# Optimization experiments

Hardware: AMD Instinct MI355X
Metric: run time of the kernel (lower is better)

Reference implementation:

```python
import jax, jax.numpy as jnp
import numpy as np

D, H, K = 384, 6, 8

def _ln(x, g, b, eps=1e-5):
    mu = jnp.mean(x, axis=-1, keepdims=True)
    var = jnp.mean((x - mu) ** 2, axis=-1, keepdims=True)
    return (x - mu) * jax.lax.rsqrt(var + eps) * g + b

def setup_inputs() -> dict:
    key = jax.random.key(0)
    ks = jax.random.split(key, 20)
    B, N = 4, 2048
    s = 0.02
    inp = {
        'x': jax.random.normal(ks[0], (B, N, D), jnp.float32),
        'knn_index': jax.random.randint(ks[1], (B * K * N,), 0, B * N, jnp.int64),
        'ln1_g': jnp.ones((D,), jnp.float32),
        'ln1_b': jnp.zeros((D,), jnp.float32),
        'w_qkv': jax.random.normal(ks[2], (D, 3 * D), jnp.float32) * s,
        'w_proj': jax.random.normal(ks[3], (D, D), jnp.float32) * s,
        'b_proj': jnp.zeros((D,), jnp.float32),
        'w_knn': jax.random.normal(ks[4], (2 * D, D), jnp.float32) * s,
        'b_knn': jnp.zeros((D,), jnp.float32),
        'w_g1': jax.random.normal(ks[5], (2 * D, D), jnp.float32) * s,
        'b_g1': jnp.zeros((D,), jnp.float32),
        'w_g2': jax.random.normal(ks[6], (D, D), jnp.float32) * s,
        'b_g2': jnp.zeros((D,), jnp.float32),
        'ln2_g': jnp.ones((D,), jnp.float32),
        'ln2_b': jnp.zeros((D,), jnp.float32),
        'w_fc1': jax.random.normal(ks[7], (D, 4 * D), jnp.float32) * s,
        'b_fc1': jnp.zeros((4 * D,), jnp.float32),
        'w_fc2': jax.random.normal(ks[8], (4 * D, D), jnp.float32) * s,
        'b_fc2': jnp.zeros((D,), jnp.float32),
    }
    return inp

def reference(x, knn_index, ln1_g, ln1_b, w_qkv, w_proj, b_proj, w_knn, b_knn,
              w_g1, b_g1, w_g2, b_g2, ln2_g, ln2_b, w_fc1, b_fc1, w_fc2, b_fc2):
    B, N, _ = x.shape
    hd = D // H
    scale = hd ** -0.5
    nx = _ln(x, ln1_g, ln1_b)
    # --- self attention ---
    qkv = (nx @ w_qkv).reshape(B, N, 3, H, hd).transpose(2, 0, 3, 1, 4)  # [3,B,H,N,hd]
    q, k, v = qkv[0], qkv[1], qkv[2]
    attn = jax.nn.softmax(jnp.einsum('bhnd,bhmd->bhnm', q * scale, k), axis=-1)
    attn_out = jnp.einsum('bhnm,bhmd->bhnd', attn, v).transpose(0, 2, 1, 3).reshape(B, N, D)
    attn_out = attn_out @ w_proj + b_proj
    # --- EdgeConv-style graph feature: gather-concat-MLP-maxpool ---
    feat = nx.reshape(B * N, D)[knn_index].reshape(B, K, N, D)
    xe = jnp.broadcast_to(nx[:, None], (B, K, N, D))
    gf = jnp.concatenate([feat - xe, xe], axis=-1)  # [B,K,N,2D]
    knn_out = jnp.max(jax.nn.leaky_relu(gf @ w_knn + b_knn, 0.2), axis=1)  # [B,N,D]
    # --- salience gate ---
    gi = jnp.concatenate([attn_out, knn_out], axis=-1)
    gate = jax.nn.sigmoid(jax.nn.gelu(gi @ w_g1 + b_g1, approximate=False) @ w_g2 + b_g2)
    fused = (1 - gate) * attn_out + gate * knn_out
    x = x + fused
    # --- FFN ---
    h = jax.nn.gelu(_ln(x, ln2_g, ln2_b) @ w_fc1 + b_fc1, approximate=False)
    x = x + (h @ w_fc2 + b_fc2)
    return x
```

## Files before the change

### kernel.cpp

```cpp
#include <hip/hip_runtime.h>
#include <math.h>

typedef unsigned short u16;
typedef __attribute__((ext_vector_type(8))) short short8;
typedef __attribute__((ext_vector_type(4))) float floatx4;
typedef __attribute__((ext_vector_type(16))) float floatx16;
typedef __attribute__((ext_vector_type(4))) short sh4v;
typedef __attribute__((ext_vector_type(2))) unsigned uint2v;

union sh4u { sh4v v; u16 u[4]; };
union sh8u { short8 v; u16 u[8]; };
union sh8w { short8 v; unsigned w[4]; };

__device__ __forceinline__ floatx4 mfma16(short8 a, short8 b, floatx4 c) {
  return __builtin_amdgcn_mfma_f32_16x16x32_bf16(a, b, c, 0, 0, 0);
}
__device__ __forceinline__ floatx16 mfma32(short8 a, short8 b, floatx16 c) {
  return __builtin_amdgcn_mfma_f32_32x32x16_bf16(a, b, c, 0, 0, 0);
}

__device__ __forceinline__ floatx4 zero4() {
  floatx4 z = {0.f, 0.f, 0.f, 0.f};
  return z;
}
__device__ __forceinline__ floatx16 zero16() {
  floatx16 z;
#pragma unroll
  for (int i = 0; i < 16; i++) z[i] = 0.f;
  return z;
}

__device__ __forceinline__ u16 f2b(float f) {
  union { float f; unsigned u; } v; v.f = f;
  unsigned u = v.u;
  return (u16)((u + 0x7FFFu + ((u >> 16) & 1u)) >> 16);
}

__device__ __forceinline__ float b2f(u16 u) {
  union { unsigned u; float f; } v; v.u = ((unsigned)u) << 16;
  return v.f;
}

__device__ __forceinline__ float blo(unsigned w) {
  union { unsigned u; float f; } v; v.u = w << 16;
  return v.f;
}
__device__ __forceinline__ float bhi(unsigned w) {
  union { unsigned u; float f; } v; v.u = w & 0xFFFF0000u;
  return v.f;
}

__device__ __forceinline__ float gelu_exact(float x) {
  return 0.5f * x * (1.f + erff(x * 0.70710678118654752440f));
}

__device__ __forceinline__ unsigned pack2(float a, float b) {
  return (unsigned)f2b(a) | ((unsigned)f2b(b) << 16);
}

__device__ __forceinline__ unsigned permpack(float p0, float p1) {
  return __builtin_amdgcn_perm(__float_as_uint(p1), __float_as_uint(p0), 0x07060302u);
}

__global__ __launch_bounds__(256) void tcln_kernel(
    const float* __restrict__ p0, const float* __restrict__ p1,
    const float* __restrict__ p2, const float* __restrict__ p3,
    const float* __restrict__ p4, const float* __restrict__ p5,
    const float* __restrict__ wknn,
    u16* __restrict__ o0, u16* __restrict__ o1, u16* __restrict__ o2,
    u16* __restrict__ o3, u16* __restrict__ o4, u16* __restrict__ o5,
    u16* __restrict__ wcT,
    const float* __restrict__ x, const float* __restrict__ g,
    const float* __restrict__ bia, u16* __restrict__ nx) {
  __shared__ u16 L[64][66];
  int t = blockIdx.x, tid = threadIdx.x;
  if (t >= 612) {
    int wave = tid >> 6, lane = tid & 63;
    int row = (t - 612) * 4 + wave;
    const float* xr = x + (size_t)row * 384;
    float v[6];
    float s = 0.f;
#pragma unroll
    for (int j = 0; j < 6; j++) { v[j] = xr[lane + 64 * j]; s += v[j]; }
#pragma unroll
    for (int off = 32; off > 0; off >>= 1) s += __shfl_xor(s, off);
    float mu = s * (1.f / 384.f);
    float ss = 0.f;
#pragma unroll
    for (int j = 0; j < 6; j++) { float d = v[j] - mu; ss += d * d; }
#pragma unroll
    for (int off = 32; off > 0; off >>= 1) ss += __shfl_xor(ss, off);
    float rstd = rsqrtf(ss * (1.f / 384.f) + 1e-5f);
    u16* orow = nx + (size_t)row * 384;
#pragma unroll
    for (int j = 0; j < 6; j++) {
      int d = lane + 64 * j;
      orow[d] = f2b((v[j] - mu) * rstd * g[d] + bia[d]);
    }
    return;
  }
  if (t >= 540) {
    t -= 540;
    int tk = t / 12, tn = t % 12;
    int k0 = tk * 64, j0 = tn * 64;
#pragma unroll
    for (int i = 0; i < 4; i++) {
      int c = tid + 256 * i;
      int r = c >> 4, c4 = (c & 15) * 4;
      floatx4 v;
      if (j0 < 384) {
        v = *(const floatx4*)(wknn + (size_t)(k0 + r) * 384 + j0 + c4);
      } else {
        floatx4 a = *(const floatx4*)(wknn + (size_t)(384 + k0 + r) * 384 + (j0 - 384) + c4);
        floatx4 b = *(const floatx4*)(wknn + (size_t)(k0 + r) * 384 + (j0 - 384) + c4);
        v = a - b;
      }
      *(unsigned*)&L[r][c4]     = pack2(v[0], v[1]);
      *(unsigned*)&L[r][c4 + 2] = pack2(v[2], v[3]);
    }
    __syncthreads();
#pragma unroll
    for (int i = 0; i < 2; i++) {
      int c = tid + 256 * i;
      int nn = c >> 3, k8 = (c & 7) * 8;
      sh8u pk;
#pragma unroll
      for (int j = 0; j < 8; j++) pk.u[j] = L[k8 + j][nn];
      *(short8*)(wcT + (size_t)(j0 + nn) * 384 + k0 + k8) = pk.v;
    }
    return;
  }
  const float* src; u16* dst; int Kd, Nd, tk, tn;
  if      (t < 108) { src = p0; dst = o0; Kd = 384;  Nd = 1152; tk = t / 18; tn = t % 18; }
  else if (t < 144) { src = p1; dst = o1; Kd = 384;  Nd = 384;  t -= 108; tk = t / 6;  tn = t % 6; }
  else if (t < 216) { src = p2; dst = o2; Kd = 768;  Nd = 384;  t -= 144; tk = t / 6;  tn = t % 6; }
  else if (t < 252) { src = p3; dst = o3; Kd = 384;  Nd = 384;  t -= 216; tk = t / 6;  tn = t % 6; }
  else if (t < 396) { src = p4; dst = o4; Kd = 384;  Nd = 1536; t -= 252; tk = t / 24; tn = t % 24; }
  else              { src = p5; dst = o5; Kd = 1536; Nd = 384;  t -= 396; tk = t / 6;  tn = t % 6; }
  int k0 = tk * 64, n0 = tn * 64;
#pragma unroll
  for (int i = 0; i < 4; i++) {
    int c = tid + 256 * i;
    int r = c >> 4, c4 = (c & 15) * 4;
    floatx4 v = *(const floatx4*)(src + (size_t)(k0 + r) * Nd + n0 + c4);
    *(unsigned*)&L[r][c4]     = pack2(v[0], v[1]);
    *(unsigned*)&L[r][c4 + 2] = pack2(v[2], v[3]);
  }
  __syncthreads();
#pragma unroll
  for (int i = 0; i < 2; i++) {
    int c = tid + 256 * i;
    int nn = c >> 3, k8 = (c & 7) * 8;
    sh8u pk;
#pragma unroll
    for (int j = 0; j < 8; j++) pk.u[j] = L[k8 + j][nn];
    *(short8*)(dst + (size_t)(n0 + nn) * Kd + k0 + k8) = pk.v;
  }
}

__global__ __launch_bounds__(256) void lnb_kernel(const u16* __restrict__ x,
                                                  const float* __restrict__ g,
                                                  const float* __restrict__ bia,
                                                  u16* __restrict__ out) {
  int wave = threadIdx.x >> 6, lane = threadIdx.x & 63;
  int row = blockIdx.x * 4 + wave;
  const u16* xr = x + (size_t)row * 384;
  float v[6];
  float s = 0.f;
#pragma unroll
  for (int j = 0; j < 6; j++) { v[j] = b2f(xr[lane + 64 * j]); s += v[j]; }
#pragma unroll
  for (int off = 32; off > 0; off >>= 1) s += __shfl_xor(s, off);
  float mu = s * (1.f / 384.f);
  float ss = 0.f;
#pragma unroll
  for (int j = 0; j < 6; j++) { float d = v[j] - mu; ss += d * d; }
#pragma unroll
  for (int off = 32; off > 0; off >>= 1) ss += __shfl_xor(ss, off);
  float rstd = rsqrtf(ss * (1.f / 384.f) + 1e-5f);
  u16* orow = out + (size_t)row * 384;
#pragma unroll
  for (int j = 0; j < 6; j++) {
    int d = lane + 64 * j;
    orow[d] = f2b((v[j] - mu) * rstd * g[d] + bia[d]);
  }
}

template <int EPI>
__global__ __launch_bounds__(256) void gemm64_kernel(
    const u16* __restrict__ A0, const u16* __restrict__ A1, int Ksplit,
    const u16* __restrict__ BwT, const u16* __restrict__ BwT2, int N, int K,
    const float* __restrict__ bias,
    float* __restrict__ outF, u16* __restrict__ outB, u16* __restrict__ outB2,
    const u16* __restrict__ eA16, const u16* __restrict__ eK16,
    const float* __restrict__ eX, u16* __restrict__ outV) {
  __shared__ u16 As[64][72];
  __shared__ u16 Bs[128][72];
  int tid = threadIdx.x;
  int lane = tid & 63, w = tid >> 6, quad = lane >> 4, l16 = lane & 15;
  int n0 = blockIdx.x * 128, m0 = blockIdx.y * 64;
  int ra = tid >> 3, ca = (tid & 7) * 8;
  const u16* Bsrc = BwT;
  int nbase = n0;
  if (EPI == 8 && n0 >= 1152) { Bsrc = BwT2; nbase = n0 - 1152; }
  floatx4 acc[4][2];
#pragma unroll
  for (int i = 0; i < 4; i++)
#pragma unroll
    for (int j = 0; j < 2; j++) acc[i][j] = zero4();

  short8 pa[2], pb[4];
  auto loadAB = [&](int k0) {
    const u16* Ap;
    int kk, sA;
    if (k0 < Ksplit) { Ap = A0; kk = k0; sA = Ksplit; }
    else             { Ap = A1; kk = k0 - Ksplit; sA = K - Ksplit; }
    pa[0] = *(const short8*)(Ap + (size_t)(m0 + ra) * sA + kk + ca);
    pa[1] = *(const short8*)(Ap + (size_t)(m0 + ra + 32) * sA + kk + ca);
#pragma unroll
    for (int i = 0; i < 4; i++)
      pb[i] = *(const short8*)(Bsrc + (size_t)(nbase + ra + 32 * i) * K + k0 + ca);
  };
  loadAB(0);
  int iters = K >> 6;
  for (int kt = 0; kt < iters; kt++) {
    __syncthreads();
    *(short8*)&As[ra][ca] = pa[0];
    *(short8*)&As[ra + 32][ca] = pa[1];
#pragma unroll
    for (int i = 0; i < 4; i++) *(short8*)&Bs[ra + 32 * i][ca] = pb[i];
    __syncthreads();
    if (kt + 1 < iters) loadAB((kt + 1) * 64);
#pragma unroll
    for (int kh = 0; kh < 2; kh++) {
      short8 af[4], bfr[2];
#pragma unroll
      for (int mt = 0; mt < 4; mt++)
        af[mt] = *(const short8*)&As[mt * 16 + l16][kh * 32 + quad * 8];
#pragma unroll
      for (int nt = 0; nt < 2; nt++)
        bfr[nt] = *(const short8*)&Bs[w * 32 + nt * 16 + l16][kh * 32 + quad * 8];
#pragma unroll
      for (int mt = 0; mt < 4; mt++)
#pragma unroll
        for (int nt = 0; nt < 2; nt++)
          acc[mt][nt] = mfma16(af[mt], bfr[nt], acc[mt][nt]);
    }
  }

#pragma unroll
  for (int mt = 0; mt < 4; mt++)
#pragma unroll
    for (int nt = 0; nt < 2; nt++) {
      int col = n0 + w * 32 + nt * 16 + l16;
      int row0 = m0 + mt * 16 + quad * 4;
      if (EPI == 8) {
        if (col < 1152) {
          float sc = (col < 384) ? 0.18033688011112042f : 1.f;
          sh4u pk;
#pragma unroll
          for (int r = 0; r < 4; r++) {
            u16 bv = f2b(acc[mt][nt][r] * sc);
            outB[(size_t)(row0 + r) * 1152 + col] = bv;
            pk.u[r] = bv;
          }
          if (col >= 768) {
            int b = row0 >> 11, n = row0 & 2047;
            int hd = col - 768;
            *(sh4v*)(outV + ((size_t)(b * 6 + (hd >> 6)) * 64 + (hd & 63)) * 2048 + n) = pk.v;
          }
        } else {
#pragma unroll
          for (int r = 0; r < 4; r++)
            outB2[(size_t)(row0 + r) * 768 + (col - 1152)] = f2b(acc[mt][nt][r]);
        }
      } else {
#pragma unroll
        for (int r = 0; r < 4; r++) {
          size_t rc = (size_t)(row0 + r) * N + col;
          float v = acc[mt][nt][r];
          if (EPI == 3) {
            outB[rc] = f2b(gelu_exact(v + bias[col]));
          } else if (EPI == 4) {
            float gte = 1.f / (1.f + __expf(-(v + bias[col])));
            float fu = (1.f - gte) * b2f(eA16[rc]) + gte * b2f(eK16[rc]);
            outB[rc] = f2b(eX[rc] + fu);
          } else if (EPI == 7) {
            outF[rc] = v + bias[col] + b2f(eA16[rc]);
          }
        }
      }
    }
}

__global__ __launch_bounds__(256) void attnknn_kernel(
    const u16* __restrict__ qkv, const u16* __restrict__ Vt,
    u16* __restrict__ OPb, float* __restrict__ LS,
    const u16* __restrict__ GBb, const int* __restrict__ kidx,
    const float* __restrict__ bknn, u16* __restrict__ knn_bf) {
  __shared__ u16 Ks[64][72];
  __shared__ u16 Vts[64][72];
  int bid = blockIdx.x, tid = threadIdx.x;
  int lane = tid & 63, w = tid >> 6;
  if (bid >= 1536) {
    int row = (bid - 1536) * 4 + w;
    int b = row >> 11, n = row & 2047;
    const unsigned* browp = (const unsigned*)(GBb + (size_t)row * 768 + 384);
    uint2v bw01 = *(const uint2v*)(browp + 2 * lane);
    unsigned bw2 = browp[128 + lane];
    floatx4 bk4 = *(const floatx4*)(bknn + 4 * lane);
    float bk40 = bknn[256 + 2 * lane], bk41 = bknn[256 + 2 * lane + 1];
    int gi[8];
#pragma unroll
    for (int kk = 0; kk < 8; kk++) gi[kk] = kidx[(b * 8 + kk) * 2048 + n];
    float mx[6];
#pragma unroll
    for (int e = 0; e < 6; e++) mx[e] = -1e30f;
#pragma unroll
    for (int kk = 0; kk < 8; kk++) {
      const unsigned* gp = (const unsigned*)(GBb + (size_t)gi[kk] * 768);
      uint2v g01 = *(const uint2v*)(gp + 2 * lane);
      unsigned g2 = gp[128 + lane];
      mx[0] = fmaxf(mx[0], blo(g01[0]));
      mx[1] = fmaxf(mx[1], bhi(g01[0]));
      mx[2] = fmaxf(mx[2], blo(g01[1]));
      mx[3] = fmaxf(mx[3], bhi(g01[1]));
      mx[4] = fmaxf(mx[4], blo(g2));
      mx[5] = fmaxf(mx[5], bhi(g2));
    }
    float vv[6];
    vv[0] = mx[0] + blo(bw01[0]) + bk4[0];
    vv[1] = mx[1] + bhi(bw01[0]) + bk4[1];
    vv[2] = mx[2] + blo(bw01[1]) + bk4[2];
    vv[3] = mx[3] + bhi(bw01[1]) + bk4[3];
    vv[4] = mx[4] + blo(bw2) + bk40;
    vv[5] = mx[5] + bhi(bw2) + bk41;
#pragma unroll
    for (int e = 0; e < 6; e++) vv[e] = fmaxf(vv[e], 0.2f * vv[e]);
    unsigned* op = (unsigned*)(knn_bf + (size_t)row * 384);
    uint2v ow;
    ow[0] = pack2(vv[0], vv[1]);
    ow[1] = pack2(vv[2], vv[3]);
    *(uint2v*)(op + 2 * lane) = ow;
    op[128 + lane] = pack2(vv[4], vv[5]);
    return;
  }
  int vb = (bid & 7) * 192 + (bid >> 3);
  int split = vb / 384;
  int rr = vb - split * 384;
  int bh = rr >> 4, b = bh / 6, h = bh % 6;
  int q0 = (rr & 15) * 128;
  int ql = lane & 31, h5 = lane >> 5;
  const u16* qbase = qkv + (size_t)b * 2048 * 1152 + h * 64;
  const u16* kbase = qbase + 384 + (size_t)split * 512 * 1152;
  const u16* vtb = Vt + (size_t)bh * 64 * 2048 + split * 512;
  int qrow = q0 + w * 32 + ql;
  short8 qB[4];
#pragma unroll
  for (int s = 0; s < 4; s++)
    qB[s] = *(const short8*)(qbase + (size_t)qrow * 1152 + s * 16 + h5 * 8);
  short8 ones;
#pragma unroll
  for (int j = 0; j < 8; j++) ones[j] = (short)0x3F80;
  floatx16 O[2];
  O[0] = zero16(); O[1] = zero16();
  floatx16 accL = zero16();

  int rb = tid >> 3, c8 = (tid & 7) * 8;
  short8 rk[2], rv[2];
  rk[0] = *(const short8*)(kbase + (size_t)rb * 1152 + c8);
  rk[1] = *(const short8*)(kbase + (size_t)(rb + 32) * 1152 + c8);
  rv[0] = *(const short8*)(vtb + (size_t)rb * 2048 + c8);
  rv[1] = *(const short8*)(vtb + (size_t)(rb + 32) * 2048 + c8);

  for (int kt = 0; kt < 8; kt++) {
    __syncthreads();
    *(short8*)&Ks[rb][c8] = rk[0];
    *(short8*)&Ks[rb + 32][c8] = rk[1];
    *(short8*)&Vts[rb][c8] = rv[0];
    *(short8*)&Vts[rb + 32][c8] = rv[1];
    __syncthreads();
    if (kt < 7) {
      int key0 = (kt + 1) * 64;
      rk[0] = *(const short8*)(kbase + (size_t)(key0 + rb) * 1152 + c8);
      rk[1] = *(const short8*)(kbase + (size_t)(key0 + rb + 32) * 1152 + c8);
      rv[0] = *(const short8*)(vtb + (size_t)rb * 2048 + key0 + c8);
      rv[1] = *(const short8*)(vtb + (size_t)(rb + 32) * 2048 + key0 + c8);
    }
#pragma unroll
    for (int t = 0; t < 2; t++) {
      floatx16 st = zero16();
#pragma unroll
      for (int s = 0; s < 4; s++) {
        short8 aK = *(const short8*)&Ks[32 * t + ql][16 * s + 8 * h5];
        st = mfma32(aK, qB[s], st);
      }
      unsigned W[8];
#pragma unroll
      for (int j = 0; j < 8; j++)
        W[j] = permpack(exp2f(st[2 * j]), exp2f(st[2 * j + 1]));
#pragma unroll
      for (int c = 0; c < 2; c++) {
        int kk = 2 * t + c;
        uint2v s0 = __builtin_amdgcn_permlane32_swap(W[4 * c], W[4 * c + 2], false, false);
        uint2v s1 = __builtin_amdgcn_permlane32_swap(W[4 * c + 1], W[4 * c + 3], false, false);
        sh8w pb_;
        pb_.w[0] = s0[0];
        pb_.w[1] = s1[0];
        pb_.w[2] = s0[1];
        pb_.w[3] = s1[1];
        accL = mfma32(ones, pb_.v, accL);
        short8 aV0 = *(const short8*)&Vts[ql][16 * kk + 8 * h5];
        short8 aV1 = *(const short8*)&Vts[32 + ql][16 * kk + 8 * h5];
        O[0] = mfma32(aV0, pb_.v, O[0]);
        O[1] = mfma32(aV1, pb_.v, O[1]);
      }
    }
  }
  u16* orow = OPb + (size_t)split * 8192 * 384 + (size_t)(b * 2048 + qrow) * 384 + h * 64;
#pragma unroll
  for (int d = 0; d < 2; d++)
#pragma unroll
    for (int rq = 0; rq < 4; rq++) {
      sh4u pk;
#pragma unroll
      for (int r3 = 0; r3 < 4; r3++) pk.u[r3] = f2b(O[d][4 * rq + r3]);
      *(sh4v*)(orow + 32 * d + 8 * rq + 4 * h5) = pk.v;
    }
  if (lane < 32) LS[split * 8192 + b * 2048 + qrow] = accL[0];
}

__global__ __launch_bounds__(256) void projc_kernel(
    const u16* __restrict__ OPb, const float* __restrict__ LS,
    const u16* __restrict__ BwT, const float* __restrict__ bias,
    u16* __restrict__ outB) {
  __shared__ u16 As[64][72];
  __shared__ u16 Bs[128][72];
  int tid = threadIdx.x;
  int lane = tid & 63, w = tid >> 6, quad = lane >> 4, l16 = lane & 15;
  int n0 = blockIdx.x * 128, m0 = blockIdx.y * 64;
  int ra = tid >> 3, ca = (tid & 7) * 8;
  const size_t SP = (size_t)8192 * 384;
  floatx4 acc[4][2];
#pragma unroll
  for (int i = 0; i < 4; i++)
#pragma unroll
    for (int j = 0; j < 2; j++) acc[i][j] = zero4();

  short8 pa[2], pb[4];
  auto loadAB = [&](int k0) {
#pragma unroll
    for (int i = 0; i < 2; i++) {
      const u16* p = OPb + (size_t)(m0 + ra + 32 * i) * 384 + k0 + ca;
      sh8u a0, a1, a2, a3, pk;
      a0.v = *(const short8*)p;
      a1.v = *(const short8*)(p + SP);
      a2.v = *(const short8*)(p + 2 * SP);
      a3.v = *(const short8*)(p + 3 * SP);
#pragma unroll
      for (int j = 0; j < 8; j++)
        pk.u[j] = f2b((b2f(a0.u[j]) + b2f(a1.u[j])) + (b2f(a2.u[j]) + b2f(a3.u[j])));
      pa[i] = pk.v;
    }
#pragma unroll
    for (int i = 0; i < 4; i++)
      pb[i] = *(const short8*)(BwT + (size_t)(n0 + ra + 32 * i) * 384 + k0 + ca);
  };
  loadAB(0);
  for (int kt = 0; kt < 6; kt++) {
    __syncthreads();
    *(short8*)&As[ra][ca] = pa[0];
    *(short8*)&As[ra + 32][ca] = pa[1];
#pragma unroll
    for (int i = 0; i < 4; i++) *(short8*)&Bs[ra + 32 * i][ca] = pb[i];
    __syncthreads();
    if (kt < 5) loadAB((kt + 1) * 64);
#pragma unroll
    for (int kh = 0; kh < 2; kh++) {
      short8 af[4], bfr[2];
#pragma unroll
      for (int mt = 0; mt < 4; mt++)
        af[mt] = *(const short8*)&As[mt * 16 + l16][kh * 32 + quad * 8];
#pragma unroll
      for (int nt = 0; nt < 2; nt++)
        bfr[nt] = *(const short8*)&Bs[w * 32 + nt * 16 + l16][kh * 32 + quad * 8];
#pragma unroll
      for (int mt = 0; mt < 4; mt++)
#pragma unroll
        for (int nt = 0; nt < 2; nt++)
          acc[mt][nt] = mfma16(af[mt], bfr[nt], acc[mt][nt]);
    }
  }
#pragma unroll
  for (int mt = 0; mt < 4; mt++) {
    int row0 = m0 + mt * 16 + quad * 4;
    float rl[4];
#pragma unroll
    for (int r = 0; r < 4; r++) {
      int gr = row0 + r;
      rl[r] = 1.f / ((LS[gr] + LS[8192 + gr]) + (LS[16384 + gr] + LS[24576 + gr]));
    }
#pragma unroll
    for (int nt = 0; nt < 2; nt++) {
      int col = n0 + w * 32 + nt * 16 + l16;
#pragma unroll
      for (int r = 0; r < 4; r++)
        outB[(size_t)(row0 + r) * 384 + col] = f2b(acc[mt][nt][r] * rl[r] + bias[col]);
    }
  }
}

extern "C" void kernel_launch(void* const* d_in, const int* in_sizes, int n_in,
                              void* d_out, int out_size, void* d_ws, size_t ws_size,
                              hipStream_t stream) {
  const float* x    = (const float*)d_in[0];
  const int* kidx   = (const int*)d_in[1];
  const float* ln1g = (const float*)d_in[2];
  const float* ln1b = (const float*)d_in[3];
  const float* wqkv = (const float*)d_in[4];
  const float* wproj= (const float*)d_in[5];
  const float* bproj= (const float*)d_in[6];
  const float* wknn = (const float*)d_in[7];
  const float* bknn = (const float*)d_in[8];
  const float* wg1  = (const float*)d_in[9];
  const float* bg1  = (const float*)d_in[10];
  const float* wg2  = (const float*)d_in[11];
  const float* bg2  = (const float*)d_in[12];
  const float* ln2g = (const float*)d_in[13];
  const float* ln2b = (const float*)d_in[14];
  const float* wfc1 = (const float*)d_in[15];
  const float* bfc1 = (const float*)d_in[16];
  const float* wfc2 = (const float*)d_in[17];
  const float* bfc2 = (const float*)d_in[18];
  float* out = (float*)d_out;

  const int M = 8192;
  char* ws = (char*)d_ws;
  size_t off = 0;
  auto alloc = [&](size_t bytes) -> char* {
    char* p = ws + off;
    off += (bytes + 255) & ~(size_t)255;
    return p;
  };
  u16* nx_bf    = (u16*)alloc((size_t)M * 384 * 2);
  u16* qkv_bf   = (u16*)alloc((size_t)M * 1152 * 2);
  u16* attn_bf  = (u16*)alloc((size_t)M * 384 * 2);
  u16* GBb      = (u16*)alloc((size_t)M * 768 * 2);
  u16* knn_bf   = (u16*)alloc((size_t)M * 384 * 2);
  u16* x2b      = (u16*)alloc((size_t)M * 384 * 2);
  u16* t1_bf    = (u16*)alloc((size_t)M * 384 * 2);
  u16* nx2_bf   = (u16*)alloc((size_t)M * 384 * 2);
  u16* Vt_b     = (u16*)alloc((size_t)24 * 64 * 2048 * 2);
  u16* OPb      = (u16*)alloc((size_t)4 * M * 384 * 2);
  float* LS     = (float*)alloc((size_t)4 * M * 4);
  u16* wqkvT    = (u16*)alloc((size_t)1152 * 384 * 2);
  u16* wprojT   = (u16*)alloc(384 * 384 * 2);
  u16* wcT      = (u16*)alloc((size_t)768 * 384 * 2);
  u16* wg1T     = (u16*)alloc((size_t)384 * 768 * 2);
  u16* wg2T     = (u16*)alloc(384 * 384 * 2);
  u16* wfc1T    = (u16*)alloc((size_t)1536 * 384 * 2);
  u16* wfc2T    = (u16*)alloc((size_t)384 * 1536 * 2);
  u16* h_bf     = qkv_bf;

  tcln_kernel<<<2660, 256, 0, stream>>>(wqkv, wproj, wg1, wg2, wfc1, wfc2, wknn,
                                        wqkvT, wprojT, wg1T, wg2T, wfc1T, wfc2T, wcT,
                                        x, ln1g, ln1b, nx_bf);
  gemm64_kernel<8><<<dim3(15, 128), 256, 0, stream>>>(nx_bf, nx_bf, 384, wqkvT, wcT, 1920, 384,
                                                      nullptr, nullptr, qkv_bf, GBb,
                                                      nullptr, nullptr, nullptr, Vt_b);
  attnknn_kernel<<<3584, 256, 0, stream>>>(qkv_bf, Vt_b, OPb, LS,
                                           GBb, kidx, bknn, knn_bf);
  projc_kernel<<<dim3(3, 128), 256, 0, stream>>>(OPb, LS, wprojT, bproj, attn_bf);
  gemm64_kernel<3><<<dim3(3, 128), 256, 0, stream>>>(attn_bf, knn_bf, 384, wg1T, nullptr, 384, 768,
                                                     bg1, nullptr, t1_bf, nullptr,
                                                     nullptr, nullptr, nullptr, nullptr);
  gemm64_kernel<4><<<dim3(3, 128), 256, 0, stream>>>(t1_bf, t1_bf, 384, wg2T, nullptr, 384, 384,
                                                     bg2, nullptr, x2b, nullptr,
                                                     attn_bf, knn_bf, x, nullptr);
  lnb_kernel<<<2048, 256, 0, stream>>>(x2b, ln2g, ln2b, nx2_bf);
  gemm64_kernel<3><<<dim3(12, 128), 256, 0, stream>>>(nx2_bf, nx2_bf, 384, wfc1T, nullptr, 1536, 384,
                                                      bfc1, nullptr, h_bf, nullptr,
                                                      nullptr, nullptr, nullptr, nullptr);
  gemm64_kernel<7><<<dim3(3, 128), 256, 0, stream>>>(h_bf, h_bf, 1536, wfc2T, nullptr, 384, 1536,
                                                     bfc2, out, nullptr, nullptr,
                                                     x2b, nullptr, nullptr, nullptr);
  (void)in_sizes; (void)n_in; (void)out_size; (void)ws_size;
}
```

Measured before the change: 267.6 us.

## Load attention K/V operands directly from global memory instead of LDS staging

The attention loop no longer stages K and V^T tiles through shared memory with double barriers. Each wave now loads its MFMA operands straight from global memory (mostly L2-resident), which removes LDS traffic and the two __syncthreads per key tile. In exchange, the four waves of a block each fetch the same K/V data redundantly, and the register prefetch that used to overlap with compute is gone, so load latency is exposed unless the compiler schedules the loads early.

```diff
diff --git a/kernel.cpp b/kernel.cpp
--- a/kernel.cpp
+++ b/kernel.cpp
@@ -298,8 +298,6 @@
     u16* __restrict__ OPb, float* __restrict__ LS,
     const u16* __restrict__ GBb, const int* __restrict__ kidx,
     const float* __restrict__ bknn, u16* __restrict__ knn_bf) {
-  __shared__ u16 Ks[64][72];
-  __shared__ u16 Vts[64][72];
   int bid = blockIdx.x, tid = threadIdx.x;
   int lane = tid & 63, w = tid >> 6;
   if (bid >= 1536) {
@@ -366,42 +364,34 @@
   O[0] = zero16(); O[1] = zero16();
   floatx16 accL = zero16();
 
-  int rb = tid >> 3, c8 = (tid & 7) * 8;
-  short8 rk[2], rv[2];
-  rk[0] = *(const short8*)(kbase + (size_t)rb * 1152 + c8);
-  rk[1] = *(const short8*)(kbase + (size_t)(rb + 32) * 1152 + c8);
-  rv[0] = *(const short8*)(vtb + (size_t)rb * 2048 + c8);
-  rv[1] = *(const short8*)(vtb + (size_t)(rb + 32) * 2048 + c8);
+  const u16* kl  = kbase + (size_t)ql * 1152 + h5 * 8;
+  const u16* vl0 = vtb + (size_t)ql * 2048 + h5 * 8;
+  const u16* vl1 = vtb + (size_t)(32 + ql) * 2048 + h5 * 8;
 
   for (int kt = 0; kt < 8; kt++) {
-    __syncthreads();
-    *(short8*)&Ks[rb][c8] = rk[0];
-    *(short8*)&Ks[rb + 32][c8] = rk[1];
-    *(short8*)&Vts[rb][c8] = rv[0];
-    *(short8*)&Vts[rb + 32][c8] = rv[1];
-    __syncthreads();
-    if (kt < 7) {
-      int key0 = (kt + 1) * 64;
-      rk[0] = *(const short8*)(kbase + (size_t)(key0 + rb) * 1152 + c8);
-      rk[1] = *(const short8*)(kbase + (size_t)(key0 + rb + 32) * 1152 + c8);
-      rv[0] = *(const short8*)(vtb + (size_t)rb * 2048 + key0 + c8);
-      rv[1] = *(const short8*)(vtb + (size_t)(rb + 32) * 2048 + key0 + c8);
-    }
 #pragma unroll
     for (int t = 0; t < 2; t++) {
+      const u16* kp = kl + (size_t)(kt * 64 + 32 * t) * 1152;
+      int vo = kt * 64 + 32 * t;
+      short8 aK0 = *(const short8*)(kp);
+      short8 aK1 = *(const short8*)(kp + 16);
+      short8 aK2 = *(const short8*)(kp + 32);
+      short8 aK3 = *(const short8*)(kp + 48);
+      short8 aV00 = *(const short8*)(vl0 + vo);
+      short8 aV10 = *(const short8*)(vl1 + vo);
+      short8 aV01 = *(const short8*)(vl0 + vo + 16);
+      short8 aV11 = *(const short8*)(vl1 + vo + 16);
       floatx16 st = zero16();
-#pragma unroll
-      for (int s = 0; s < 4; s++) {
-        short8 aK = *(const short8*)&Ks[32 * t + ql][16 * s + 8 * h5];
-        st = mfma32(aK, qB[s], st);
-      }
+      st = mfma32(aK0, qB[0], st);
+      st = mfma32(aK1, qB[1], st);
+      st = mfma32(aK2, qB[2], st);
+      st = mfma32(aK3, qB[3], st);
       unsigned W[8];
 #pragma unroll
       for (int j = 0; j < 8; j++)
         W[j] = permpack(exp2f(st[2 * j]), exp2f(st[2 * j + 1]));
 #pragma unroll
       for (int c = 0; c < 2; c++) {
-        int kk = 2 * t + c;
         uint2v s0 = __builtin_amdgcn_permlane32_swap(W[4 * c], W[4 * c + 2], false, false);
         uint2v s1 = __builtin_amdgcn_permlane32_swap(W[4 * c + 1], W[4 * c + 3], false, false);
         sh8w pb_;
@@ -410,10 +400,8 @@
         pb_.w[2] = s0[1];
         pb_.w[3] = s1[1];
         accL = mfma32(ones, pb_.v, accL);
-        short8 aV0 = *(const short8*)&Vts[ql][16 * kk + 8 * h5];
-        short8 aV1 = *(const short8*)&Vts[32 + ql][16 * kk + 8 * h5];
-        O[0] = mfma32(aV0, pb_.v, O[0]);
-        O[1] = mfma32(aV1, pb_.v, O[1]);
+        O[0] = mfma32(c ? aV01 : aV00, pb_.v, O[0]);
+        O[1] = mfma32(c ? aV11 : aV10, pb_.v, O[1]);
       }
     }
   }
```

New measurement: 317.6 us. 1.19x slower.
